# Performance work log

Measured on AMD Instinct MI355X. Metric: run time of the kernel, lower is better.

The kernel has to match this reference:

```python
import jax, jax.numpy as jnp
import numpy as np

N = 50000       # nodes
E = 500000      # edges
F_IN = 64       # input feature dim
F_OUT = 64      # hidden/output dim
K = 3           # diffusion filter order
C = F_IN + F_OUT  # concat dim seen by each DConv


def _xavier(k, shape):
    fan_in, fan_out = shape[-2], shape[-1]
    lim = float(np.sqrt(6.0 / (fan_in + fan_out)))
    return jax.random.uniform(k, shape, jnp.float32, -lim, lim)


def setup_inputs() -> dict:
    key = jax.random.key(0)
    ks = jax.random.split(key, 8)
    X = jax.random.normal(ks[0], (N, F_IN), jnp.float32)
    H = jax.random.normal(ks[1], (N, F_OUT), jnp.float32)
    # ring edges guarantee every node has in-degree >= 1 and out-degree >= 1
    base = jnp.arange(N, dtype=jnp.int32)
    row = jnp.concatenate([base, jax.random.randint(ks[2], (E - N,), 0, N, jnp.int32)])
    col = jnp.concatenate([jnp.roll(base, 1), jax.random.randint(ks[3], (E - N,), 0, N, jnp.int32)])
    edge_index = jnp.stack([row, col])  # [2, E]
    W_z = _xavier(ks[4], (2, K, C, F_OUT))
    W_r = _xavier(ks[5], (2, K, C, F_OUT))
    W_h = _xavier(ks[6], (2, K, C, F_OUT))
    b = jnp.zeros((F_OUT,), jnp.float32)
    return {"X": X, "edge_index": edge_index, "H": H,
            "W_z": W_z, "b_z": b, "W_r": W_r, "b_r": b, "W_h": W_h, "b_h": b}


def _dconv(Xc, row, col, norm_out, norm_in, W, b):
    # PyG propagate: gather source (row) features, scale by edge norm, scatter-add to target (col)
    def prop(x, norm):
        return jax.ops.segment_sum(norm[:, None] * x[row], col, num_segments=N)
    Tx_0 = Xc
    Hout = Xc @ (W[0, 0] + W[1, 0])
    Tx_1_o = prop(Xc, norm_out)
    Tx_1_i = prop(Xc, norm_in)
    Hout = Hout + Tx_1_o @ W[0, 1] + Tx_1_i @ W[1, 1]
    for k in range(2, K):
        Tx_2_o = 2.0 * prop(Tx_1_o, norm_out) - Tx_0
        Tx_2_i = 2.0 * prop(Tx_1_i, norm_in) - Tx_0
        Hout = Hout + Tx_2_o @ W[0, k] + Tx_2_i @ W[1, k]
        # faithful to original: Tx_1 is never reassigned, so Tx_0 stays Xc
        Tx_0, Tx_1_o, Tx_1_i = Xc, Tx_2_o, Tx_2_i
    return Hout + b


def reference(X, edge_index, H, W_z, b_z, W_r, b_r, W_h, b_h):
    row, col = edge_index[0], edge_index[1]
    deg_out = jnp.zeros((N,), jnp.float32).at[row].add(1.0)
    deg_in = jnp.zeros((N,), jnp.float32).at[col].add(1.0)
    norm_out = (1.0 / deg_out)[row]
    norm_in = (1.0 / deg_in)[row]
    XH = jnp.concatenate([X, H], axis=1)
    Z = jax.nn.sigmoid(_dconv(XH, row, col, norm_out, norm_in, W_z, b_z))
    R = jax.nn.sigmoid(_dconv(XH, row, col, norm_out, norm_in, W_r, b_r))
    XHR = jnp.concatenate([X, H * R], axis=1)
    H_tilde = jnp.tanh(_dconv(XHR, row, col, norm_out, norm_in, W_h, b_h))
    H_new = Z * H + (1.0 - Z) * H_tilde
    # NaN infill with mean of non-NaN entries (faithful to original)
    mask = jnp.isnan(H_new)
    H_new = jnp.where(mask, jnp.nanmean(H_new), H_new)
    return H_new
```

## Files before the change

### kernel.cpp

```cpp
#include <hip/hip_runtime.h>
#include <hip/hip_bf16.h>
#include <math.h>

#define N_NODES 50000
#define N_EDGES 500000
#define C_DIM 128
#define N_TILES 3125

typedef __attribute__((ext_vector_type(8))) short bf8;
typedef __attribute__((ext_vector_type(4))) float f32x4;

__device__ __forceinline__ float bflo(unsigned u) { return __uint_as_float(u << 16); }
__device__ __forceinline__ float bfhi(unsigned u) { return __uint_as_float(u & 0xffff0000u); }
__device__ __forceinline__ unsigned short f2bfu(float f) {
    __hip_bfloat16 h = __float2bfloat16(f);
    unsigned short u;
    __builtin_memcpy(&u, &h, 2);
    return u;
}
__device__ __forceinline__ unsigned packbf(float a, float b) {
    return ((unsigned)f2bfu(b) << 16) | f2bfu(a);
}


__global__ void count_deg(const int* __restrict__ row, const int* __restrict__ col,
                          int* __restrict__ dout, int* __restrict__ din, int e) {
    int i = blockIdx.x * blockDim.x + threadIdx.x;
    if (i >= e) return;
    atomicAdd(&dout[row[i]], 1);
    atomicAdd(&din[col[i]], 1);
}

__global__ void scan_block(const int* __restrict__ counts, int* __restrict__ excl,
                           int* __restrict__ blocksums, int n) {
    __shared__ int tmp[1024];
    int tid = threadIdx.x;
    int gid = blockIdx.x * 1024 + tid;
    int v = (gid < n) ? counts[gid] : 0;
    tmp[tid] = v;
    __syncthreads();
    for (int off = 1; off < 1024; off <<= 1) {
        int t = (tid >= off) ? tmp[tid - off] : 0;
        __syncthreads();
        tmp[tid] += t;
        __syncthreads();
    }
    int incl = tmp[tid];
    if (gid < n) excl[gid] = incl - v;
    if (tid == 1023) blocksums[blockIdx.x] = incl;
}

__global__ void scan_sums(int* __restrict__ blocksums, int nb) {
    __shared__ int tmp[64];
    int tid = threadIdx.x;
    int v = (tid < nb) ? blocksums[tid] : 0;
    tmp[tid] = v;
    __syncthreads();
    for (int off = 1; off < 64; off <<= 1) {
        int t = (tid >= off) ? tmp[tid - off] : 0;
        __syncthreads();
        tmp[tid] += t;
        __syncthreads();
    }
    if (tid < nb) blocksums[tid] = tmp[tid] - v;
}

__global__ void scan_add(int* __restrict__ rowptr, const int* __restrict__ blocksums,
                         int* __restrict__ cursor, const int* __restrict__ dout,
                         const int* __restrict__ din, float2* __restrict__ winv,
                         int n, int e_total) {
    int gid = blockIdx.x * blockDim.x + threadIdx.x;
    if (gid < n) {
        int v = rowptr[gid] + blocksums[gid >> 10];
        rowptr[gid] = v;
        cursor[gid] = v;
        winv[gid] = make_float2(1.0f / (float)dout[gid], 1.0f / (float)din[gid]);
    }
    if (gid == n) rowptr[n] = e_total;
}

__global__ void build_csr(const int* __restrict__ row, const int* __restrict__ col,
                          const float2* __restrict__ winv,
                          int* __restrict__ cursor, int* __restrict__ src,
                          float2* __restrict__ w, int e) {
    int i = blockIdx.x * blockDim.x + threadIdx.x;
    if (i >= e) return;
    int r = row[i], c = col[i];
    int pos = atomicAdd(&cursor[c], 1);
    src[pos] = r;
    w[pos] = winv[r];
}

__device__ __forceinline__ float wraw(const float* W, int d, int kk, int k, int j) {
    return W[((d * 3 + kk) * 128 + k) * 64 + j];
}

__device__ __forceinline__ float zr_val(const float* Wz, const float* Wr, int k, int nn) {
    const float* W = (nn < 64) ? Wz : Wr;
    int j = nn & 63;
    if (k < 128) return wraw(W, 0, 0, k, j) + wraw(W, 1, 0, k, j);
    int k2 = k - 128;
    int kk = (k2 >= 256) ? 2 : 1;
    int k3 = k2 & 255;
    int p = k3 >> 2, sub = k3 & 3;
    return wraw(W, sub >> 1, kk, 2 * p + (sub & 1), j);
}

__device__ __forceinline__ float h_val(const float* Wh, int k, int j) {
    if (k < 64) return wraw(Wh, 0, 0, k, j) + wraw(Wh, 1, 0, k, j);
    if (k < 320) {
        int k2 = k - 64;
        int kk = (k2 >= 128) ? 2 : 1;
        int k3 = k2 & 127;
        int p = k3 >> 2, sub = k3 & 3;
        return wraw(Wh, sub >> 1, kk, 2 * p + (sub & 1), j);
    }
    if (k < 384) return wraw(Wh, 0, 0, 64 + (k - 320), j) + wraw(Wh, 1, 0, 64 + (k - 320), j);
    int k2 = k - 384;
    int kk = (k2 >= 128) ? 2 : 1;
    int k3 = k2 & 127;
    int p = k3 >> 2, sub = k3 & 3;
    return wraw(Wh, sub >> 1, kk, 64 + 2 * p + (sub & 1), j);
}

__global__ void pack_weights(const float* __restrict__ Wz, const float* __restrict__ Wr,
                             const float* __restrict__ Wh,
                             unsigned short* __restrict__ Wzrf,
                             unsigned short* __restrict__ Whf) {
    int i = blockIdx.x * blockDim.x + threadIdx.x;
    if (i < 20 * 8 * 64 * 8) {
        int j = i & 7, lane = (i >> 3) & 63, nt = (i >> 9) & 7, ks = i >> 12;
        int k = ks * 32 + (lane >> 4) * 8 + j;
        int nn = nt * 16 + (lane & 15);
        Wzrf[i] = f2bfu(zr_val(Wz, Wr, k, nn));
    } else if (i < 20 * 8 * 64 * 8 + 20 * 4 * 64 * 8) {
        int i2 = i - 20 * 8 * 64 * 8;
        int j = i2 & 7, lane = (i2 >> 3) & 63, nt = (i2 >> 9) & 3, ks = i2 >> 11;
        int k = ks * 32 + (lane >> 4) * 8 + j;
        int nn = nt * 16 + (lane & 15);
        Whf[i2] = f2bfu(h_val(Wh, k, nn));
    }
}


__global__ void concat_xh(const float* __restrict__ X, const float* __restrict__ H,
                          unsigned short* __restrict__ XH, unsigned short* __restrict__ XHp,
                          int n) {
    int t = blockIdx.x * blockDim.x + threadIdx.x;
    if (t >= n * 16) return;
    int node = t >> 4, p = t & 15;
    const float* src = (p < 8) ? (X + (size_t)node * 64 + 8 * p)
                               : (H + (size_t)node * 64 + 8 * (p - 8));
    float4 v0 = *(const float4*)src;
    float4 v1 = *(const float4*)(src + 4);
    uint4 o;
    o.x = packbf(v0.x, v0.y); o.y = packbf(v0.z, v0.w);
    o.z = packbf(v1.x, v1.y); o.w = packbf(v1.z, v1.w);
    *(uint4*)(XH + (size_t)node * 128 + 8 * p) = o;
    int tile = node >> 4, lr = node & 15, ck = p >> 2, q = p & 3;
    *(uint4*)(XHp + (((size_t)tile * 4 + ck) * 64 + q * 16 + lr) * 8) = o;
}


__global__ void prop1_128(const unsigned short* __restrict__ S,
                          const int* __restrict__ rowptr, const int* __restrict__ src,
                          const float2* __restrict__ w,
                          unsigned short* __restrict__ P1, unsigned short* __restrict__ P1p,
                          int n) {
    int tid = blockIdx.x * blockDim.x + threadIdx.x;
    int lane = tid & 63;
    int node = ((tid >> 6) << 1) + (lane >> 5);
    int p = lane & 31;
    if (node >= n) return;
    int beg = rowptr[node], end = rowptr[node + 1];
    float ao0 = 0.f, ao1 = 0.f, ao2 = 0.f, ao3 = 0.f;
    float ai0 = 0.f, ai1 = 0.f, ai2 = 0.f, ai3 = 0.f;
    int j = beg;
#define P1STEP(s_, w_) {                                                     \
        uint2 u = *(const uint2*)(S + (size_t)(s_) * 128 + 4 * p);           \
        float c0 = bflo(u.x), c1 = bfhi(u.x), c2 = bflo(u.y), c3 = bfhi(u.y);\
        ao0 = fmaf(w_.x, c0, ao0); ao1 = fmaf(w_.x, c1, ao1);                \
        ao2 = fmaf(w_.x, c2, ao2); ao3 = fmaf(w_.x, c3, ao3);                \
        ai0 = fmaf(w_.y, c0, ai0); ai1 = fmaf(w_.y, c1, ai1);                \
        ai2 = fmaf(w_.y, c2, ai2); ai3 = fmaf(w_.y, c3, ai3); }
    for (; j + 4 <= end; j += 4) {
        int s0 = src[j], s1 = src[j + 1], s2 = src[j + 2], s3 = src[j + 3];
        float2 w0 = w[j], w1 = w[j + 1], w2 = w[j + 2], w3 = w[j + 3];
        P1STEP(s0, w0); P1STEP(s1, w1); P1STEP(s2, w2); P1STEP(s3, w3);
    }
    for (; j < end; ++j) {
        int s = src[j]; float2 wv = w[j];
        P1STEP(s, wv);
    }
#undef P1STEP
    uint4 o;
    o.x = packbf(ao0, ao1); o.y = packbf(ai0, ai1);
    o.z = packbf(ao2, ao3); o.w = packbf(ai2, ai3);
    *(uint4*)(P1 + (size_t)node * 256 + 8 * p) = o;
    int tile = node >> 4, lr = node & 15, ck = p >> 2, q = p & 3;
    *(uint4*)(P1p + (((size_t)tile * 8 + ck) * 64 + q * 16 + lr) * 8) = o;
}

__global__ void prop2_128(const unsigned short* __restrict__ P1,
                          const unsigned short* __restrict__ Xc,
                          const int* __restrict__ rowptr, const int* __restrict__ src,
                          const float2* __restrict__ w,
                          unsigned short* __restrict__ P2p, int n) {
    int tid = blockIdx.x * blockDim.x + threadIdx.x;
    int lane = tid & 63;
    int node = ((tid >> 6) << 1) + (lane >> 5);
    int p = lane & 31;
    if (node >= n) return;
    int beg = rowptr[node], end = rowptr[node + 1];
    float oa = 0.f, ob = 0.f, oc = 0.f, od = 0.f;
    float ia = 0.f, ib = 0.f, ic = 0.f, id = 0.f;
    int j = beg;
#define P2STEP(s_, w_) {                                                     \
        uint4 v = *(const uint4*)(P1 + (size_t)(s_) * 256 + 8 * p);          \
        oa = fmaf(w_.x, bflo(v.x), oa); ob = fmaf(w_.x, bfhi(v.x), ob);      \
        ia = fmaf(w_.y, bflo(v.y), ia); ib = fmaf(w_.y, bfhi(v.y), ib);      \
        oc = fmaf(w_.x, bflo(v.z), oc); od = fmaf(w_.x, bfhi(v.z), od);      \
        ic = fmaf(w_.y, bflo(v.w), ic); id = fmaf(w_.y, bfhi(v.w), id); }
    for (; j + 4 <= end; j += 4) {
        int s0 = src[j], s1 = src[j + 1], s2 = src[j + 2], s3 = src[j + 3];
        float2 w0 = w[j], w1 = w[j + 1], w2 = w[j + 2], w3 = w[j + 3];
        P2STEP(s0, w0); P2STEP(s1, w1); P2STEP(s2, w2); P2STEP(s3, w3);
    }
    for (; j < end; ++j) {
        int s = src[j]; float2 wv = w[j];
        P2STEP(s, wv);
    }
#undef P2STEP
    uint2 ux = *(const uint2*)(Xc + (size_t)node * 128 + 4 * p);
    float xa = bflo(ux.x), xb = bfhi(ux.x), xc = bflo(ux.y), xd = bfhi(ux.y);
    uint4 o;
    o.x = packbf(2.f * oa - xa, 2.f * ob - xb);
    o.y = packbf(2.f * ia - xa, 2.f * ib - xb);
    o.z = packbf(2.f * oc - xc, 2.f * od - xd);
    o.w = packbf(2.f * ic - xc, 2.f * id - xd);
    int tile = node >> 4, lr = node & 15, ck = p >> 2, q = p & 3;
    *(uint4*)(P2p + (((size_t)tile * 8 + ck) * 64 + q * 16 + lr) * 8) = o;
}

__global__ void prop1_64(const unsigned short* __restrict__ HR,
                         const int* __restrict__ rowptr, const int* __restrict__ src,
                         const float2* __restrict__ w,
                         unsigned short* __restrict__ Q1, unsigned short* __restrict__ Q1p,
                         int n) {
    int tid = blockIdx.x * blockDim.x + threadIdx.x;
    int lane = tid & 63;
    int node = ((tid >> 6) << 2) + (lane >> 4);
    int p = lane & 15;
    if (node >= n) return;
    int beg = rowptr[node], end = rowptr[node + 1];
    float ao0 = 0.f, ao1 = 0.f, ao2 = 0.f, ao3 = 0.f;
    float ai0 = 0.f, ai1 = 0.f, ai2 = 0.f, ai3 = 0.f;
    int j = beg;
#define Q1STEP(s_, w_) {                                                     \
        uint2 u = *(const uint2*)(HR + (size_t)(s_) * 64 + 4 * p);           \
        float c0 = bflo(u.x), c1 = bfhi(u.x), c2 = bflo(u.y), c3 = bfhi(u.y);\
        ao0 = fmaf(w_.x, c0, ao0); ao1 = fmaf(w_.x, c1, ao1);                \
        ao2 = fmaf(w_.x, c2, ao2); ao3 = fmaf(w_.x, c3, ao3);                \
        ai0 = fmaf(w_.y, c0, ai0); ai1 = fmaf(w_.y, c1, ai1);                \
        ai2 = fmaf(w_.y, c2, ai2); ai3 = fmaf(w_.y, c3, ai3); }
    for (; j + 4 <= end; j += 4) {
        int s0 = src[j], s1 = src[j + 1], s2 = src[j + 2], s3 = src[j + 3];
        float2 w0 = w[j], w1 = w[j + 1], w2 = w[j + 2], w3 = w[j + 3];
        Q1STEP(s0, w0); Q1STEP(s1, w1); Q1STEP(s2, w2); Q1STEP(s3, w3);
    }
    for (; j < end; ++j) {
        int s = src[j]; float2 wv = w[j];
        Q1STEP(s, wv);
    }
#undef Q1STEP
    uint4 o;
    o.x = packbf(ao0, ao1); o.y = packbf(ai0, ai1);
    o.z = packbf(ao2, ao3); o.w = packbf(ai2, ai3);
    *(uint4*)(Q1 + (size_t)node * 128 + 8 * p) = o;
    int tile = node >> 4, lr = node & 15, ck = p >> 2, q = p & 3;
    *(uint4*)(Q1p + (((size_t)tile * 4 + ck) * 64 + q * 16 + lr) * 8) = o;
}

__global__ void prop2_64(const unsigned short* __restrict__ Q1,
                         const unsigned short* __restrict__ HR,
                         const int* __restrict__ rowptr, const int* __restrict__ src,
                         const float2* __restrict__ w,
                         unsigned short* __restrict__ Q2p, int n) {
    int tid = blockIdx.x * blockDim.x + threadIdx.x;
    int lane = tid & 63;
    int node = ((tid >> 6) << 2) + (lane >> 4);
    int p = lane & 15;
    if (node >= n) return;
    int beg = rowptr[node], end = rowptr[node + 1];
    float oa = 0.f, ob = 0.f, oc = 0.f, od = 0.f;
    float ia = 0.f, ib = 0.f, ic = 0.f, id = 0.f;
    int j = beg;
#define Q2STEP(s_, w_) {                                                     \
        uint4 v = *(const uint4*)(Q1 + (size_t)(s_) * 128 + 8 * p);          \
        oa = fmaf(w_.x, bflo(v.x), oa); ob = fmaf(w_.x, bfhi(v.x), ob);      \
        ia = fmaf(w_.y, bflo(v.y), ia); ib = fmaf(w_.y, bfhi(v.y), ib);      \
        oc = fmaf(w_.x, bflo(v.z), oc); od = fmaf(w_.x, bfhi(v.z), od);      \
        ic = fmaf(w_.y, bflo(v.w), ic); id = fmaf(w_.y, bfhi(v.w), id); }
    for (; j + 4 <= end; j += 4) {
        int s0 = src[j], s1 = src[j + 1], s2 = src[j + 2], s3 = src[j + 3];
        float2 w0 = w[j], w1 = w[j + 1], w2 = w[j + 2], w3 = w[j + 3];
        Q2STEP(s0, w0); Q2STEP(s1, w1); Q2STEP(s2, w2); Q2STEP(s3, w3);
    }
    for (; j < end; ++j) {
        int s = src[j]; float2 wv = w[j];
        Q2STEP(s, wv);
    }
#undef Q2STEP
    uint2 ux = *(const uint2*)(HR + (size_t)node * 64 + 4 * p);
    float xa = bflo(ux.x), xb = bfhi(ux.x), xc = bflo(ux.y), xd = bfhi(ux.y);
    uint4 o;
    o.x = packbf(2.f * oa - xa, 2.f * ob - xb);
    o.y = packbf(2.f * ia - xa, 2.f * ib - xb);
    o.z = packbf(2.f * oc - xc, 2.f * od - xd);
    o.w = packbf(2.f * ic - xc, 2.f * id - xd);
    int tile = node >> 4, lr = node & 15, ck = p >> 2, q = p & 3;
    *(uint4*)(Q2p + (((size_t)tile * 4 + ck) * 64 + q * 16 + lr) * 8) = o;
}


__global__ __launch_bounds__(256) void gemm_zr_mfma(
    const unsigned short* __restrict__ XHp, const unsigned short* __restrict__ P1p,
    const unsigned short* __restrict__ P2p,
    const unsigned short* __restrict__ Wf, const float* __restrict__ bz,
    const float* __restrict__ br, const float* __restrict__ H,
    float* __restrict__ Zf, unsigned short* __restrict__ HR, int n) {
    int tid = threadIdx.x;
    int lane = tid & 63;
    int ngrp = tid >> 6;
    int rowbase = blockIdx.x * 64;
    int lr = lane & 15, quad = lane >> 4;

    int tiles[4];
#pragma unroll
    for (int mt = 0; mt < 4; ++mt) {
        int t = (rowbase >> 4) + mt;
        tiles[mt] = (t > N_TILES - 1) ? N_TILES - 1 : t;
    }

    f32x4 zero = {0.f, 0.f, 0.f, 0.f};
    f32x4 acc[4][2];
#pragma unroll
    for (int a = 0; a < 4; ++a)
#pragma unroll
        for (int b = 0; b < 2; ++b) acc[a][b] = zero;

#pragma unroll
    for (int ks = 0; ks < 20; ++ks) {
        const unsigned short* T = (ks < 4) ? XHp : (ks < 12) ? P1p : P2p;
        int ck = (ks < 4) ? ks : (ks < 12) ? ks - 4 : ks - 12;
        int nck = (ks < 4) ? 4 : 8;
        bf8 b0 = *(const bf8*)(Wf + (((size_t)ks * 8 + ngrp * 2 + 0) * 64 + lane) * 8);
        bf8 b1 = *(const bf8*)(Wf + (((size_t)ks * 8 + ngrp * 2 + 1) * 64 + lane) * 8);
#pragma unroll
        for (int mt = 0; mt < 4; ++mt) {
            bf8 a = *(const bf8*)(T + (((size_t)tiles[mt] * nck + ck) * 64 + lane) * 8);
            acc[mt][0] = __builtin_amdgcn_mfma_f32_16x16x32_bf16(a, b0, acc[mt][0], 0, 0, 0);
            acc[mt][1] = __builtin_amdgcn_mfma_f32_16x16x32_bf16(a, b1, acc[mt][1], 0, 0, 0);
        }
    }
#pragma unroll
    for (int mt = 0; mt < 4; ++mt)
#pragma unroll
        for (int reg = 0; reg < 4; ++reg) {
            int r = rowbase + mt * 16 + quad * 4 + reg;
            if (r >= n) continue;
#pragma unroll
            for (int nt = 0; nt < 2; ++nt) {
                int cidx = ngrp * 32 + nt * 16 + lr;
                float bias = (cidx < 64) ? bz[cidx] : br[cidx - 64];
                float v = acc[mt][nt][reg] + bias;
                float s = 1.f / (1.f + expf(-v));
                if (cidx < 64) {
                    Zf[(size_t)r * 64 + cidx] = s;
                } else {
                    int c2 = cidx - 64;
                    HR[(size_t)r * 64 + c2] = f2bfu(H[(size_t)r * 64 + c2] * s);
                }
            }
        }
}

__global__ __launch_bounds__(256) void gemm_h_mfma(
    const unsigned short* __restrict__ XHp, const unsigned short* __restrict__ P1p,
    const unsigned short* __restrict__ P2p, const unsigned short* __restrict__ HR,
    const unsigned short* __restrict__ Q1p, const unsigned short* __restrict__ Q2p,
    const unsigned short* __restrict__ Wf, const float* __restrict__ bh,
    const float* __restrict__ Zf, const float* __restrict__ H,
    float* __restrict__ out, int n) {
    int tid = threadIdx.x;
    int lane = tid & 63;
    int wid = tid >> 6;
    int mh = wid & 1, ngrp = wid >> 1;
    int rowbase = blockIdx.x * 128 + mh * 64;
    int lr = lane & 15, quad = lane >> 4;

    int tiles[4];
    const unsigned short* hrp[4];
#pragma unroll
    for (int mt = 0; mt < 4; ++mt) {
        int t = (rowbase >> 4) + mt;
        tiles[mt] = (t > N_TILES - 1) ? N_TILES - 1 : t;
        int r = rowbase + mt * 16 + lr;
        if (r >= n) r = n - 1;
        hrp[mt] = HR + (size_t)r * 64 + quad * 8;
    }

    f32x4 zero = {0.f, 0.f, 0.f, 0.f};
    f32x4 acc[4][2];
#pragma unroll
    for (int a = 0; a < 4; ++a)
#pragma unroll
        for (int b = 0; b < 2; ++b) acc[a][b] = zero;

#pragma unroll
    for (int ks = 0; ks < 20; ++ks) {
        bf8 b0 = *(const bf8*)(Wf + (((size_t)ks * 4 + ngrp * 2 + 0) * 64 + lane) * 8);
        bf8 b1 = *(const bf8*)(Wf + (((size_t)ks * 4 + ngrp * 2 + 1) * 64 + lane) * 8);
#pragma unroll
        for (int mt = 0; mt < 4; ++mt) {
            bf8 a;
            if (ks == 10 || ks == 11) {
                a = *(const bf8*)(hrp[mt] + (ks - 10) * 32);
            } else {
                const unsigned short* T = (ks < 2) ? XHp : (ks < 6) ? P1p :
                                          (ks < 10) ? P2p : (ks < 16) ? Q1p : Q2p;
                int ck = (ks < 2) ? ks : (ks < 6) ? ks - 2 : (ks < 10) ? ks - 6 :
                         (ks < 16) ? ks - 12 : ks - 16;
                int nck = (ks < 2) ? 4 : (ks < 10) ? 8 : 4;
                a = *(const bf8*)(T + (((size_t)tiles[mt] * nck + ck) * 64 + lane) * 8);
            }
            acc[mt][0] = __builtin_amdgcn_mfma_f32_16x16x32_bf16(a, b0, acc[mt][0], 0, 0, 0);
            acc[mt][1] = __builtin_amdgcn_mfma_f32_16x16x32_bf16(a, b1, acc[mt][1], 0, 0, 0);
        }
    }
#pragma unroll
    for (int mt = 0; mt < 4; ++mt)
#pragma unroll
        for (int reg = 0; reg < 4; ++reg) {
            int r = rowbase + mt * 16 + quad * 4 + reg;
            if (r >= n) continue;
#pragma unroll
            for (int nt = 0; nt < 2; ++nt) {
                int cidx = ngrp * 32 + nt * 16 + lr;
                float ht = tanhf(acc[mt][nt][reg] + bh[cidx]);
                float z = Zf[(size_t)r * 64 + cidx];
                float h_old = H[(size_t)r * 64 + cidx];
                out[(size_t)r * 64 + cidx] = z * h_old + (1.f - z) * ht;
            }
        }
}


static inline size_t rup(size_t x) { return (x + 63) & ~(size_t)63; }

extern "C" void kernel_launch(void* const* d_in, const int* in_sizes, int n_in,
                              void* d_out, int out_size, void* d_ws, size_t ws_size,
                              hipStream_t stream) {
    const float* X  = (const float*)d_in[0];
    const int*   EI = (const int*)d_in[1];
    const float* H  = (const float*)d_in[2];
    const float* Wz = (const float*)d_in[3];
    const float* bz = (const float*)d_in[4];
    const float* Wr = (const float*)d_in[5];
    const float* br = (const float*)d_in[6];
    const float* Wh = (const float*)d_in[7];
    const float* bh = (const float*)d_in[8];
    float* out = (float*)d_out;

    const int* row = EI;
    const int* col = EI + N_EDGES;

    char* ws = (char*)d_ws;
    size_t off = 0;
    auto carve = [&](size_t bytes) { void* p = ws + off; off += rup(bytes); return p; };

    int*   deg_out   = (int*)carve(N_NODES * 4);
    int*   deg_in    = (int*)carve(N_NODES * 4);
    int*   rowptr    = (int*)carve((N_NODES + 1) * 4);
    int*   cursor    = (int*)carve(N_NODES * 4);
    int*   blocksums = (int*)carve(64 * 4);
    float2* winv     = (float2*)carve(N_NODES * 8);
    int*   csr_src   = (int*)carve(N_EDGES * 4);
    float2* csr_w    = (float2*)carve(N_EDGES * 8);
    unsigned short* XH  = (unsigned short*)carve((size_t)N_NODES * 128 * 2);
    unsigned short* P1  = (unsigned short*)carve((size_t)N_NODES * 256 * 2);
    unsigned short* XHp = (unsigned short*)carve((size_t)N_TILES * 4 * 512 * 2);
    unsigned short* P1p = (unsigned short*)carve((size_t)N_TILES * 8 * 512 * 2);
    unsigned short* P2p = (unsigned short*)carve((size_t)N_TILES * 8 * 512 * 2);
    unsigned short* HR  = (unsigned short*)carve((size_t)N_NODES * 64 * 2);
    float* Zf           = (float*)carve((size_t)N_NODES * 64 * 4);
    unsigned short* Wzrf = (unsigned short*)carve(20 * 8 * 64 * 8 * 2);
    unsigned short* Whf  = (unsigned short*)carve(20 * 4 * 64 * 8 * 2);

    unsigned short* Q1  = XH;
    unsigned short* Q1p = P1;
    unsigned short* Q2p = P1 + (size_t)N_TILES * 4 * 512;

    hipMemsetAsync(deg_out, 0, rup(N_NODES * 4) + rup(N_NODES * 4), stream);
    count_deg<<<(N_EDGES + 255) / 256, 256, 0, stream>>>(row, col, deg_out, deg_in, N_EDGES);

    int nblk = (N_NODES + 1023) / 1024;
    scan_block<<<nblk, 1024, 0, stream>>>(deg_in, rowptr, blocksums, N_NODES);
    scan_sums<<<1, 64, 0, stream>>>(blocksums, nblk);
    scan_add<<<(N_NODES + 1 + 255) / 256, 256, 0, stream>>>(rowptr, blocksums, cursor,
                                                            deg_out, deg_in, winv, N_NODES, N_EDGES);

    build_csr<<<(N_EDGES + 255) / 256, 256, 0, stream>>>(row, col, winv, cursor,
                                                         csr_src, csr_w, N_EDGES);

    pack_weights<<<(20 * 8 * 64 * 8 + 20 * 4 * 64 * 8 + 255) / 256, 256, 0, stream>>>(
        Wz, Wr, Wh, Wzrf, Whf);

    concat_xh<<<(N_NODES * 16 + 255) / 256, 256, 0, stream>>>(X, H, XH, XHp, N_NODES);

    int blocks_p128 = (((N_NODES + 1) / 2) * 64 + 255) / 256;
    prop1_128<<<blocks_p128, 256, 0, stream>>>(XH, rowptr, csr_src, csr_w, P1, P1p, N_NODES);
    prop2_128<<<blocks_p128, 256, 0, stream>>>(P1, XH, rowptr, csr_src, csr_w, P2p, N_NODES);

    int zr_blocks = (N_NODES + 63) / 64;
    gemm_zr_mfma<<<zr_blocks, 256, 0, stream>>>(XHp, P1p, P2p, Wzrf, bz, br, H, Zf, HR, N_NODES);

    int blocks_p64 = (((N_NODES + 3) / 4) * 64 + 255) / 256;
    prop1_64<<<blocks_p64, 256, 0, stream>>>(HR, rowptr, csr_src, csr_w, Q1, Q1p, N_NODES);
    prop2_64<<<blocks_p64, 256, 0, stream>>>(Q1, HR, rowptr, csr_src, csr_w, Q2p, N_NODES);

    int h_blocks = (N_NODES + 127) / 128;
    gemm_h_mfma<<<h_blocks, 256, 0, stream>>>(XHp, P1p, P2p, HR, Q1p, Q2p,
                                              Whf, bh, Zf, H, out, N_NODES);
}
```

Baseline: 369.4 us.

## Fuse second-hop propagation into MFMA GEMMs via LDS and merge prep kernels

The second-order diffusion propagation is now computed inside the GEMM kernels: each block gathers its own rows' second hop into shared memory and feeds MFMA from LDS. This removes the P2/Q2 global round trips and two launches. The CSR build, concat and weight packing kernels are merged into one launch, and the first-hop gather loops are unrolled by 8. In exchange, the GEMM blocks now carry a latency-bound gather phase before the MFMA phase, which may hurt occupancy and overlap. A partial P2 copy (the X part only) is still written globally for reuse in the H GEMM.

Measured after the change: 377.3 us. +2.1%, slower.

```diff
diff --git a/kernel.cpp b/kernel.cpp
--- a/kernel.cpp
+++ b/kernel.cpp
@@ -6,6 +6,10 @@
 #define N_EDGES 500000
 #define C_DIM 128
 #define N_TILES 3125
+
+#define CSR_BLOCKS 1954
+#define CONCAT_BLOCKS 3125
+#define PACK_BLOCKS 480
 
 typedef __attribute__((ext_vector_type(8))) short bf8;
 typedef __attribute__((ext_vector_type(4))) float f32x4;
@@ -79,18 +83,6 @@
     if (gid == n) rowptr[n] = e_total;
 }
 
-__global__ void build_csr(const int* __restrict__ row, const int* __restrict__ col,
-                          const float2* __restrict__ winv,
-                          int* __restrict__ cursor, int* __restrict__ src,
-                          float2* __restrict__ w, int e) {
-    int i = blockIdx.x * blockDim.x + threadIdx.x;
-    if (i >= e) return;
-    int r = row[i], c = col[i];
-    int pos = atomicAdd(&cursor[c], 1);
-    src[pos] = r;
-    w[pos] = winv[r];
-}
-
 __device__ __forceinline__ float wraw(const float* W, int d, int kk, int k, int j) {
     return W[((d * 3 + kk) * 128 + k) * 64 + j];
 }
@@ -123,42 +115,51 @@
     return wraw(Wh, sub >> 1, kk, 64 + 2 * p + (sub & 1), j);
 }
 
-__global__ void pack_weights(const float* __restrict__ Wz, const float* __restrict__ Wr,
-                             const float* __restrict__ Wh,
-                             unsigned short* __restrict__ Wzrf,
-                             unsigned short* __restrict__ Whf) {
-    int i = blockIdx.x * blockDim.x + threadIdx.x;
-    if (i < 20 * 8 * 64 * 8) {
-        int j = i & 7, lane = (i >> 3) & 63, nt = (i >> 9) & 7, ks = i >> 12;
-        int k = ks * 32 + (lane >> 4) * 8 + j;
-        int nn = nt * 16 + (lane & 15);
-        Wzrf[i] = f2bfu(zr_val(Wz, Wr, k, nn));
-    } else if (i < 20 * 8 * 64 * 8 + 20 * 4 * 64 * 8) {
-        int i2 = i - 20 * 8 * 64 * 8;
-        int j = i2 & 7, lane = (i2 >> 3) & 63, nt = (i2 >> 9) & 3, ks = i2 >> 11;
-        int k = ks * 32 + (lane >> 4) * 8 + j;
-        int nn = nt * 16 + (lane & 15);
-        Whf[i2] = f2bfu(h_val(Wh, k, nn));
-    }
-}
-
-
-__global__ void concat_xh(const float* __restrict__ X, const float* __restrict__ H,
-                          unsigned short* __restrict__ XH, unsigned short* __restrict__ XHp,
-                          int n) {
-    int t = blockIdx.x * blockDim.x + threadIdx.x;
-    if (t >= n * 16) return;
-    int node = t >> 4, p = t & 15;
-    const float* src = (p < 8) ? (X + (size_t)node * 64 + 8 * p)
-                               : (H + (size_t)node * 64 + 8 * (p - 8));
-    float4 v0 = *(const float4*)src;
-    float4 v1 = *(const float4*)(src + 4);
-    uint4 o;
-    o.x = packbf(v0.x, v0.y); o.y = packbf(v0.z, v0.w);
-    o.z = packbf(v1.x, v1.y); o.w = packbf(v1.z, v1.w);
-    *(uint4*)(XH + (size_t)node * 128 + 8 * p) = o;
-    int tile = node >> 4, lr = node & 15, ck = p >> 2, q = p & 3;
-    *(uint4*)(XHp + (((size_t)tile * 4 + ck) * 64 + q * 16 + lr) * 8) = o;
+__global__ void fused_prep(const int* __restrict__ row, const int* __restrict__ col,
+                           const float2* __restrict__ winv, int* __restrict__ cursor,
+                           int* __restrict__ csr_src, float2* __restrict__ csr_w,
+                           const float* __restrict__ X, const float* __restrict__ Hm,
+                           unsigned short* __restrict__ XH, unsigned short* __restrict__ XHp,
+                           const float* __restrict__ Wz, const float* __restrict__ Wr,
+                           const float* __restrict__ Wh,
+                           unsigned short* __restrict__ Wzrf, unsigned short* __restrict__ Whf,
+                           int n, int e) {
+    int b = blockIdx.x;
+    if (b < CSR_BLOCKS) {
+        int i = b * 256 + threadIdx.x;
+        if (i >= e) return;
+        int r = row[i], c = col[i];
+        int pos = atomicAdd(&cursor[c], 1);
+        csr_src[pos] = r;
+        csr_w[pos] = winv[r];
+    } else if (b < CSR_BLOCKS + CONCAT_BLOCKS) {
+        int t = (b - CSR_BLOCKS) * 256 + threadIdx.x;
+        int node = t >> 4, p = t & 15;
+        const float* src = (p < 8) ? (X + (size_t)node * 64 + 8 * p)
+                                   : (Hm + (size_t)node * 64 + 8 * (p - 8));
+        float4 v0 = *(const float4*)src;
+        float4 v1 = *(const float4*)(src + 4);
+        uint4 o;
+        o.x = packbf(v0.x, v0.y); o.y = packbf(v0.z, v0.w);
+        o.z = packbf(v1.x, v1.y); o.w = packbf(v1.z, v1.w);
+        *(uint4*)(XH + (size_t)node * 128 + 8 * p) = o;
+        int tile = node >> 4, lr = node & 15, ck = p >> 2, q = p & 3;
+        *(uint4*)(XHp + (((size_t)tile * 4 + ck) * 64 + q * 16 + lr) * 8) = o;
+    } else {
+        int i = (b - CSR_BLOCKS - CONCAT_BLOCKS) * 256 + threadIdx.x;
+        if (i < 20 * 8 * 64 * 8) {
+            int j = i & 7, lane = (i >> 3) & 63, nt = (i >> 9) & 7, ks = i >> 12;
+            int k = ks * 32 + (lane >> 4) * 8 + j;
+            int nn = nt * 16 + (lane & 15);
+            Wzrf[i] = f2bfu(zr_val(Wz, Wr, k, nn));
+        } else if (i < 20 * 8 * 64 * 8 + 20 * 4 * 64 * 8) {
+            int i2 = i - 20 * 8 * 64 * 8;
+            int j = i2 & 7, lane = (i2 >> 3) & 63, nt = (i2 >> 9) & 3, ks = i2 >> 11;
+            int k = ks * 32 + (lane >> 4) * 8 + j;
+            int nn = nt * 16 + (lane & 15);
+            Whf[i2] = f2bfu(h_val(Wh, k, nn));
+        }
+    }
 }
 
 
@@ -183,6 +184,14 @@
         ao2 = fmaf(w_.x, c2, ao2); ao3 = fmaf(w_.x, c3, ao3);                \
         ai0 = fmaf(w_.y, c0, ai0); ai1 = fmaf(w_.y, c1, ai1);                \
         ai2 = fmaf(w_.y, c2, ai2); ai3 = fmaf(w_.y, c3, ai3); }
+    for (; j + 8 <= end; j += 8) {
+        int s0 = src[j], s1 = src[j + 1], s2 = src[j + 2], s3 = src[j + 3];
+        int s4 = src[j + 4], s5 = src[j + 5], s6 = src[j + 6], s7 = src[j + 7];
+        float2 w0 = w[j], w1 = w[j + 1], w2 = w[j + 2], w3 = w[j + 3];
+        float2 w4 = w[j + 4], w5 = w[j + 5], w6 = w[j + 6], w7 = w[j + 7];
+        P1STEP(s0, w0); P1STEP(s1, w1); P1STEP(s2, w2); P1STEP(s3, w3);
+        P1STEP(s4, w4); P1STEP(s5, w5); P1STEP(s6, w6); P1STEP(s7, w7);
+    }
     for (; j + 4 <= end; j += 4) {
         int s0 = src[j], s1 = src[j + 1], s2 = src[j + 2], s3 = src[j + 3];
         float2 w0 = w[j], w1 = w[j + 1], w2 = w[j + 2], w3 = w[j + 3];
@@ -199,47 +208,6 @@
     *(uint4*)(P1 + (size_t)node * 256 + 8 * p) = o;
     int tile = node >> 4, lr = node & 15, ck = p >> 2, q = p & 3;
     *(uint4*)(P1p + (((size_t)tile * 8 + ck) * 64 + q * 16 + lr) * 8) = o;
-}
-
-__global__ void prop2_128(const unsigned short* __restrict__ P1,
-                          const unsigned short* __restrict__ Xc,
-                          const int* __restrict__ rowptr, const int* __restrict__ src,
-                          const float2* __restrict__ w,
-                          unsigned short* __restrict__ P2p, int n) {
-    int tid = blockIdx.x * blockDim.x + threadIdx.x;
-    int lane = tid & 63;
-    int node = ((tid >> 6) << 1) + (lane >> 5);
-    int p = lane & 31;
-    if (node >= n) return;
-    int beg = rowptr[node], end = rowptr[node + 1];
-    float oa = 0.f, ob = 0.f, oc = 0.f, od = 0.f;
-    float ia = 0.f, ib = 0.f, ic = 0.f, id = 0.f;
-    int j = beg;
-#define P2STEP(s_, w_) {                                                     \
-        uint4 v = *(const uint4*)(P1 + (size_t)(s_) * 256 + 8 * p);          \
-        oa = fmaf(w_.x, bflo(v.x), oa); ob = fmaf(w_.x, bfhi(v.x), ob);      \
-        ia = fmaf(w_.y, bflo(v.y), ia); ib = fmaf(w_.y, bfhi(v.y), ib);      \
-        oc = fmaf(w_.x, bflo(v.z), oc); od = fmaf(w_.x, bfhi(v.z), od);      \
-        ic = fmaf(w_.y, bflo(v.w), ic); id = fmaf(w_.y, bfhi(v.w), id); }
-    for (; j + 4 <= end; j += 4) {
-        int s0 = src[j], s1 = src[j + 1], s2 = src[j + 2], s3 = src[j + 3];
-        float2 w0 = w[j], w1 = w[j + 1], w2 = w[j + 2], w3 = w[j + 3];
-        P2STEP(s0, w0); P2STEP(s1, w1); P2STEP(s2, w2); P2STEP(s3, w3);
-    }
-    for (; j < end; ++j) {
-        int s = src[j]; float2 wv = w[j];
-        P2STEP(s, wv);
-    }
-#undef P2STEP
-    uint2 ux = *(const uint2*)(Xc + (size_t)node * 128 + 4 * p);
-    float xa = bflo(ux.x), xb = bfhi(ux.x), xc = bflo(ux.y), xd = bfhi(ux.y);
-    uint4 o;
-    o.x = packbf(2.f * oa - xa, 2.f * ob - xb);
-    o.y = packbf(2.f * ia - xa, 2.f * ib - xb);
-    o.z = packbf(2.f * oc - xc, 2.f * od - xd);
-    o.w = packbf(2.f * ic - xc, 2.f * id - xd);
-    int tile = node >> 4, lr = node & 15, ck = p >> 2, q = p & 3;
-    *(uint4*)(P2p + (((size_t)tile * 8 + ck) * 64 + q * 16 + lr) * 8) = o;
 }
 
 __global__ void prop1_64(const unsigned short* __restrict__ HR,
@@ -263,6 +231,14 @@
         ao2 = fmaf(w_.x, c2, ao2); ao3 = fmaf(w_.x, c3, ao3);                \
         ai0 = fmaf(w_.y, c0, ai0); ai1 = fmaf(w_.y, c1, ai1);                \
         ai2 = fmaf(w_.y, c2, ai2); ai3 = fmaf(w_.y, c3, ai3); }
+    for (; j + 8 <= end; j += 8) {
+        int s0 = src[j], s1 = src[j + 1], s2 = src[j + 2], s3 = src[j + 3];
+        int s4 = src[j + 4], s5 = src[j + 5], s6 = src[j + 6], s7 = src[j + 7];
+        float2 w0 = w[j], w1 = w[j + 1], w2 = w[j + 2], w3 = w[j + 3];
+        float2 w4 = w[j + 4], w5 = w[j + 5], w6 = w[j + 6], w7 = w[j + 7];
+        Q1STEP(s0, w0); Q1STEP(s1, w1); Q1STEP(s2, w2); Q1STEP(s3, w3);
+        Q1STEP(s4, w4); Q1STEP(s5, w5); Q1STEP(s6, w6); Q1STEP(s7, w7);
+    }
     for (; j + 4 <= end; j += 4) {
         int s0 = src[j], s1 = src[j + 1], s2 = src[j + 2], s3 = src[j + 3];
         float2 w0 = w[j], w1 = w[j + 1], w2 = w[j + 2], w3 = w[j + 3];
@@ -281,60 +257,66 @@
     *(uint4*)(Q1p + (((size_t)tile * 4 + ck) * 64 + q * 16 + lr) * 8) = o;
 }
 
-__global__ void prop2_64(const unsigned short* __restrict__ Q1,
-                         const unsigned short* __restrict__ HR,
-                         const int* __restrict__ rowptr, const int* __restrict__ src,
-                         const float2* __restrict__ w,
-                         unsigned short* __restrict__ Q2p, int n) {
-    int tid = blockIdx.x * blockDim.x + threadIdx.x;
+
+__global__ __launch_bounds__(256) void prop2_gemm_zr(
+    const unsigned short* __restrict__ P1, const unsigned short* __restrict__ Xc,
+    const int* __restrict__ rowptr, const int* __restrict__ src,
+    const float2* __restrict__ w,
+    const unsigned short* __restrict__ XHp, const unsigned short* __restrict__ P1p,
+    unsigned short* __restrict__ P2xp,
+    const unsigned short* __restrict__ Wf, const float* __restrict__ bz,
+    const float* __restrict__ br, const float* __restrict__ H,
+    float* __restrict__ Zf, unsigned short* __restrict__ HR, int n) {
+    __shared__ unsigned short P2l[32 * 65 * 8];
+    int tid = threadIdx.x;
     int lane = tid & 63;
-    int node = ((tid >> 6) << 2) + (lane >> 4);
-    int p = lane & 15;
-    if (node >= n) return;
-    int beg = rowptr[node], end = rowptr[node + 1];
-    float oa = 0.f, ob = 0.f, oc = 0.f, od = 0.f;
-    float ia = 0.f, ib = 0.f, ic = 0.f, id = 0.f;
-    int j = beg;
-#define Q2STEP(s_, w_) {                                                     \
-        uint4 v = *(const uint4*)(Q1 + (size_t)(s_) * 128 + 8 * p);          \
+    int wid = tid >> 6;
+    int rowbase = blockIdx.x * 64;
+    int half = lane >> 5, p = lane & 31;
+
+    for (int iter = 0; iter < 8; ++iter) {
+        int nl = wid * 16 + iter * 2 + half;
+        int node = rowbase + nl;
+        uint4 o = make_uint4(0u, 0u, 0u, 0u);
+        if (node < n) {
+            int beg = rowptr[node], end = rowptr[node + 1];
+            float oa = 0.f, ob = 0.f, oc = 0.f, od = 0.f;
+            float ia = 0.f, ib = 0.f, ic = 0.f, id = 0.f;
+            int j = beg;
+#define P2STEP(s_, w_) {                                                     \
+        uint4 v = *(const uint4*)(P1 + (size_t)(s_) * 256 + 8 * p);          \
         oa = fmaf(w_.x, bflo(v.x), oa); ob = fmaf(w_.x, bfhi(v.x), ob);      \
         ia = fmaf(w_.y, bflo(v.y), ia); ib = fmaf(w_.y, bfhi(v.y), ib);      \
         oc = fmaf(w_.x, bflo(v.z), oc); od = fmaf(w_.x, bfhi(v.z), od);      \
         ic = fmaf(w_.y, bflo(v.w), ic); id = fmaf(w_.y, bfhi(v.w), id); }
-    for (; j + 4 <= end; j += 4) {
-        int s0 = src[j], s1 = src[j + 1], s2 = src[j + 2], s3 = src[j + 3];
-        float2 w0 = w[j], w1 = w[j + 1], w2 = w[j + 2], w3 = w[j + 3];
-        Q2STEP(s0, w0); Q2STEP(s1, w1); Q2STEP(s2, w2); Q2STEP(s3, w3);
-    }
-    for (; j < end; ++j) {
-        int s = src[j]; float2 wv = w[j];
-        Q2STEP(s, wv);
-    }
-#undef Q2STEP
-    uint2 ux = *(const uint2*)(HR + (size_t)node * 64 + 4 * p);
-    float xa = bflo(ux.x), xb = bfhi(ux.x), xc = bflo(ux.y), xd = bfhi(ux.y);
-    uint4 o;
-    o.x = packbf(2.f * oa - xa, 2.f * ob - xb);
-    o.y = packbf(2.f * ia - xa, 2.f * ib - xb);
-    o.z = packbf(2.f * oc - xc, 2.f * od - xd);
-    o.w = packbf(2.f * ic - xc, 2.f * id - xd);
-    int tile = node >> 4, lr = node & 15, ck = p >> 2, q = p & 3;
-    *(uint4*)(Q2p + (((size_t)tile * 4 + ck) * 64 + q * 16 + lr) * 8) = o;
-}
-
-
-__global__ __launch_bounds__(256) void gemm_zr_mfma(
-    const unsigned short* __restrict__ XHp, const unsigned short* __restrict__ P1p,
-    const unsigned short* __restrict__ P2p,
-    const unsigned short* __restrict__ Wf, const float* __restrict__ bz,
-    const float* __restrict__ br, const float* __restrict__ H,
-    float* __restrict__ Zf, unsigned short* __restrict__ HR, int n) {
-    int tid = threadIdx.x;
-    int lane = tid & 63;
-    int ngrp = tid >> 6;
-    int rowbase = blockIdx.x * 64;
+            for (; j + 4 <= end; j += 4) {
+                int s0 = src[j], s1 = src[j + 1], s2 = src[j + 2], s3 = src[j + 3];
+                float2 w0 = w[j], w1 = w[j + 1], w2 = w[j + 2], w3 = w[j + 3];
+                P2STEP(s0, w0); P2STEP(s1, w1); P2STEP(s2, w2); P2STEP(s3, w3);
+            }
+            for (; j < end; ++j) {
+                int s = src[j]; float2 wv = w[j];
+                P2STEP(s, wv);
+            }
+#undef P2STEP
+            uint2 ux = *(const uint2*)(Xc + (size_t)node * 128 + 4 * p);
+            float xa = bflo(ux.x), xb = bfhi(ux.x), xc2 = bflo(ux.y), xd = bfhi(ux.y);
+            o.x = packbf(2.f * oa - xa, 2.f * ob - xb);
+            o.y = packbf(2.f * ia - xa, 2.f * ib - xb);
+            o.z = packbf(2.f * oc - xc2, 2.f * od - xd);
+            o.w = packbf(2.f * ic - xc2, 2.f * id - xd);
+        }
+        int mtile = nl >> 4, lr = nl & 15, ck = p >> 2, q = p & 3;
+        *(uint4*)&P2l[((mtile * 8 + ck) * 65 + q * 16 + lr) * 8] = o;
+        if (ck < 4 && node < n) {
+            int gtile = node >> 4;
+            *(uint4*)(P2xp + (((size_t)gtile * 4 + ck) * 64 + q * 16 + lr) * 8) = o;
+        }
+    }
+    __syncthreads();
+
+    int ngrp = wid;
     int lr = lane & 15, quad = lane >> 4;
-
     int tiles[4];
 #pragma unroll
     for (int mt = 0; mt < 4; ++mt) {
@@ -351,14 +333,18 @@
 
 #pragma unroll
     for (int ks = 0; ks < 20; ++ks) {
-        const unsigned short* T = (ks < 4) ? XHp : (ks < 12) ? P1p : P2p;
-        int ck = (ks < 4) ? ks : (ks < 12) ? ks - 4 : ks - 12;
-        int nck = (ks < 4) ? 4 : 8;
         bf8 b0 = *(const bf8*)(Wf + (((size_t)ks * 8 + ngrp * 2 + 0) * 64 + lane) * 8);
         bf8 b1 = *(const bf8*)(Wf + (((size_t)ks * 8 + ngrp * 2 + 1) * 64 + lane) * 8);
 #pragma unroll
         for (int mt = 0; mt < 4; ++mt) {
-            bf8 a = *(const bf8*)(T + (((size_t)tiles[mt] * nck + ck) * 64 + lane) * 8);
+            bf8 a;
+            if (ks < 4) {
+                a = *(const bf8*)(XHp + (((size_t)tiles[mt] * 4 + ks) * 64 + lane) * 8);
+            } else if (ks < 12) {
+                a = *(const bf8*)(P1p + (((size_t)tiles[mt] * 8 + (ks - 4)) * 64 + lane) * 8);
+            } else {
+                a = *(const bf8*)&P2l[((mt * 8 + (ks - 12)) * 65 + lane) * 8];
+            }
             acc[mt][0] = __builtin_amdgcn_mfma_f32_16x16x32_bf16(a, b0, acc[mt][0], 0, 0, 0);
             acc[mt][1] = __builtin_amdgcn_mfma_f32_16x16x32_bf16(a, b1, acc[mt][1], 0, 0, 0);
         }
@@ -385,27 +371,69 @@
         }
 }
 
-__global__ __launch_bounds__(256) void gemm_h_mfma(
+__global__ __launch_bounds__(256) void prop2_gemm_h(
+    const unsigned short* __restrict__ Q1, const unsigned short* __restrict__ HR,
+    const int* __restrict__ rowptr, const int* __restrict__ src,
+    const float2* __restrict__ w,
     const unsigned short* __restrict__ XHp, const unsigned short* __restrict__ P1p,
-    const unsigned short* __restrict__ P2p, const unsigned short* __restrict__ HR,
-    const unsigned short* __restrict__ Q1p, const unsigned short* __restrict__ Q2p,
+    const unsigned short* __restrict__ P2xp, const unsigned short* __restrict__ Q1p,
     const unsigned short* __restrict__ Wf, const float* __restrict__ bh,
     const float* __restrict__ Zf, const float* __restrict__ H,
     float* __restrict__ out, int n) {
+    __shared__ unsigned short Q2l[32 * 65 * 8];
     int tid = threadIdx.x;
     int lane = tid & 63;
     int wid = tid >> 6;
+    int rowbase = blockIdx.x * 128;
+    int quarter = lane >> 4, p = lane & 15;
+
+    for (int iter = 0; iter < 8; ++iter) {
+        int nl = wid * 32 + iter * 4 + quarter;
+        int node = rowbase + nl;
+        uint4 o = make_uint4(0u, 0u, 0u, 0u);
+        if (node < n) {
+            int beg = rowptr[node], end = rowptr[node + 1];
+            float oa = 0.f, ob = 0.f, oc = 0.f, od = 0.f;
+            float ia = 0.f, ib = 0.f, ic = 0.f, id = 0.f;
+            int j = beg;
+#define Q2STEP(s_, w_) {                                                     \
+        uint4 v = *(const uint4*)(Q1 + (size_t)(s_) * 128 + 8 * p);          \
+        oa = fmaf(w_.x, bflo(v.x), oa); ob = fmaf(w_.x, bfhi(v.x), ob);      \
+        ia = fmaf(w_.y, bflo(v.y), ia); ib = fmaf(w_.y, bfhi(v.y), ib);      \
+        oc = fmaf(w_.x, bflo(v.z), oc); od = fmaf(w_.x, bfhi(v.z), od);      \
+        ic = fmaf(w_.y, bflo(v.w), ic); id = fmaf(w_.y, bfhi(v.w), id); }
+            for (; j + 4 <= end; j += 4) {
+                int s0 = src[j], s1 = src[j + 1], s2 = src[j + 2], s3 = src[j + 3];
+                float2 w0 = w[j], w1 = w[j + 1], w2 = w[j + 2], w3 = w[j + 3];
+                Q2STEP(s0, w0); Q2STEP(s1, w1); Q2STEP(s2, w2); Q2STEP(s3, w3);
+            }
+            for (; j < end; ++j) {
+                int s = src[j]; float2 wv = w[j];
+                Q2STEP(s, wv);
+            }
+#undef Q2STEP
+            uint2 ux = *(const uint2*)(HR + (size_t)node * 64 + 4 * p);
+            float xa = bflo(ux.x), xb = bfhi(ux.x), xc2 = bflo(ux.y), xd = bfhi(ux.y);
+            o.x = packbf(2.f * oa - xa, 2.f * ob - xb);
+            o.y = packbf(2.f * ia - xa, 2.f * ib - xb);
+            o.z = packbf(2.f * oc - xc2, 2.f * od - xd);
+            o.w = packbf(2.f * ic - xc2, 2.f * id - xd);
+        }
+        int mtile = nl >> 4, lr = nl & 15, ck = p >> 2, q = p & 3;
+        *(uint4*)&Q2l[((mtile * 4 + ck) * 65 + q * 16 + lr) * 8] = o;
+    }
+    __syncthreads();
+
     int mh = wid & 1, ngrp = wid >> 1;
-    int rowbase = blockIdx.x * 128 + mh * 64;
+    int rb = rowbase + mh * 64;
     int lr = lane & 15, quad = lane >> 4;
-
     int tiles[4];
     const unsigned short* hrp[4];
 #pragma unroll
     for (int mt = 0; mt < 4; ++mt) {
-        int t = (rowbase >> 4) + mt;
+        int t = (rb >> 4) + mt;
         tiles[mt] = (t > N_TILES - 1) ? N_TILES - 1 : t;
-        int r = rowbase + mt * 16 + lr;
+        int r = rb + mt * 16 + lr;
         if (r >= n) r = n - 1;
         hrp[mt] = HR + (size_t)r * 64 + quad * 8;
     }
@@ -424,15 +452,18 @@
 #pragma unroll
         for (int mt = 0; mt < 4; ++mt) {
             bf8 a;
-            if (ks == 10 || ks == 11) {
+            if (ks < 2) {
+                a = *(const bf8*)(XHp + (((size_t)tiles[mt] * 4 + ks) * 64 + lane) * 8);
+            } else if (ks < 6) {
+                a = *(const bf8*)(P1p + (((size_t)tiles[mt] * 8 + (ks - 2)) * 64 + lane) * 8);
+            } else if (ks < 10) {
+                a = *(const bf8*)(P2xp + (((size_t)tiles[mt] * 4 + (ks - 6)) * 64 + lane) * 8);
+            } else if (ks < 12) {
                 a = *(const bf8*)(hrp[mt] + (ks - 10) * 32);
+            } else if (ks < 16) {
+                a = *(const bf8*)(Q1p + (((size_t)tiles[mt] * 4 + (ks - 12)) * 64 + lane) * 8);
             } else {
-                const unsigned short* T = (ks < 2) ? XHp : (ks < 6) ? P1p :
-                                          (ks < 10) ? P2p : (ks < 16) ? Q1p : Q2p;
-                int ck = (ks < 2) ? ks : (ks < 6) ? ks - 2 : (ks < 10) ? ks - 6 :
-                         (ks < 16) ? ks - 12 : ks - 16;
-                int nck = (ks < 2) ? 4 : (ks < 10) ? 8 : 4;
-                a = *(const bf8*)(T + (((size_t)tiles[mt] * nck + ck) * 64 + lane) * 8);
+                a = *(const bf8*)&Q2l[(((mh * 4 + mt) * 4 + (ks - 16)) * 65 + lane) * 8];
             }
             acc[mt][0] = __builtin_amdgcn_mfma_f32_16x16x32_bf16(a, b0, acc[mt][0], 0, 0, 0);
             acc[mt][1] = __builtin_amdgcn_mfma_f32_16x16x32_bf16(a, b1, acc[mt][1], 0, 0, 0);
@@ -442,7 +473,7 @@
     for (int mt = 0; mt < 4; ++mt)
 #pragma unroll
         for (int reg = 0; reg < 4; ++reg) {
-            int r = rowbase + mt * 16 + quad * 4 + reg;
+            int r = rb + mt * 16 + quad * 4 + reg;
             if (r >= n) continue;
 #pragma unroll
             for (int nt = 0; nt < 2; ++nt) {
@@ -491,7 +522,7 @@
     unsigned short* P1  = (unsigned short*)carve((size_t)N_NODES * 256 * 2);
     unsigned short* XHp = (unsigned short*)carve((size_t)N_TILES * 4 * 512 * 2);
     unsigned short* P1p = (unsigned short*)carve((size_t)N_TILES * 8 * 512 * 2);
-    unsigned short* P2p = (unsigned short*)carve((size_t)N_TILES * 8 * 512 * 2);
+    unsigned short* P2xp = (unsigned short*)carve((size_t)N_TILES * 4 * 512 * 2);
     unsigned short* HR  = (unsigned short*)carve((size_t)N_NODES * 64 * 2);
     float* Zf           = (float*)carve((size_t)N_NODES * 64 * 4);
     unsigned short* Wzrf = (unsigned short*)carve(20 * 8 * 64 * 8 * 2);
@@ -499,7 +530,6 @@
 
     unsigned short* Q1  = XH;
     unsigned short* Q1p = P1;
-    unsigned short* Q2p = P1 + (size_t)N_TILES * 4 * 512;
 
     hipMemsetAsync(deg_out, 0, rup(N_NODES * 4) + rup(N_NODES * 4), stream);
     count_deg<<<(N_EDGES + 255) / 256, 256, 0, stream>>>(row, col, deg_out, deg_in, N_EDGES);
@@ -510,26 +540,23 @@
     scan_add<<<(N_NODES + 1 + 255) / 256, 256, 0, stream>>>(rowptr, blocksums, cursor,
                                                             deg_out, deg_in, winv, N_NODES, N_EDGES);
 
-    build_csr<<<(N_EDGES + 255) / 256, 256, 0, stream>>>(row, col, winv, cursor,
-                                                         csr_src, csr_w, N_EDGES);
-
-    pack_weights<<<(20 * 8 * 64 * 8 + 20 * 4 * 64 * 8 + 255) / 256, 256, 0, stream>>>(
-        Wz, Wr, Wh, Wzrf, Whf);
-
-    concat_xh<<<(N_NODES * 16 + 255) / 256, 256, 0, stream>>>(X, H, XH, XHp, N_NODES);
+    fused_prep<<<CSR_BLOCKS + CONCAT_BLOCKS + PACK_BLOCKS, 256, 0, stream>>>(
+        row, col, winv, cursor, csr_src, csr_w,
+        X, H, XH, XHp, Wz, Wr, Wh, Wzrf, Whf, N_NODES, N_EDGES);
 
     int blocks_p128 = (((N_NODES + 1) / 2) * 64 + 255) / 256;
     prop1_128<<<blocks_p128, 256, 0, stream>>>(XH, rowptr, csr_src, csr_w, P1, P1p, N_NODES);
-    prop2_128<<<blocks_p128, 256, 0, stream>>>(P1, XH, rowptr, csr_src, csr_w, P2p, N_NODES);
 
     int zr_blocks = (N_NODES + 63) / 64;
-    gemm_zr_mfma<<<zr_blocks, 256, 0, stream>>>(XHp, P1p, P2p, Wzrf, bz, br, H, Zf, HR, N_NODES);
+    prop2_gemm_zr<<<zr_blocks, 256, 0, stream>>>(P1, XH, rowptr, csr_src, csr_w,
+                                                 XHp, P1p, P2xp, Wzrf, bz, br, H,
+                                                 Zf, HR, N_NODES);
 
     int blocks_p64 = (((N_NODES + 3) / 4) * 64 + 255) / 256;
     prop1_64<<<blocks_p64, 256, 0, stream>>>(HR, rowptr, csr_src, csr_w, Q1, Q1p, N_NODES);
-    prop2_64<<<blocks_p64, 256, 0, stream>>>(Q1, HR, rowptr, csr_src, csr_w, Q2p, N_NODES);
 
     int h_blocks = (N_NODES + 127) / 128;
-    gemm_h_mfma<<<h_blocks, 256, 0, stream>>>(XHp, P1p, P2p, HR, Q1p, Q2p,
-                                              Whf, bh, Zf, H, out, N_NODES);
-}
+    prop2_gemm_h<<<h_blocks, 256, 0, stream>>>(Q1, HR, rowptr, csr_src, csr_w,
+                                               XHp, P1p, P2xp, Q1p, Whf, bh,
+                                               Zf, H, out, N_NODES);
+}
```
